# Kernel optimization log

Hardware: AMD Instinct MI355X
Metric: run time of the kernel (lower is better)

## Reference

```python
import jax, jax.numpy as jnp
import numpy as np

CH = 256
C8 = CH // 8


def setup_inputs() -> dict:
    key = jax.random.key(0)
    ks = jax.random.split(key, 8)
    scale = 1.0 / np.sqrt(CH)
    x = jax.random.normal(ks[0], (8, CH, 64, 64), dtype=jnp.float32)
    Wq = jax.random.normal(ks[1], (C8, CH), dtype=jnp.float32) * scale
    bq = jnp.zeros((C8,), dtype=jnp.float32)
    Wk = jax.random.normal(ks[2], (C8, CH), dtype=jnp.float32) * scale
    bk = jnp.zeros((C8,), dtype=jnp.float32)
    Wv = jax.random.normal(ks[3], (CH, CH), dtype=jnp.float32) * scale
    bv = jnp.zeros((CH,), dtype=jnp.float32)
    gamma = jnp.full((1,), 0.1, dtype=jnp.float32)  # nonzero so output depends on attention path
    return {"x": x, "Wq": Wq, "bq": bq, "Wk": Wk, "bk": bk, "Wv": Wv, "bv": bv, "gamma": gamma}


def reference(x, Wq, bq, Wk, bk, Wv, bv, gamma):
    b, c, h, w = x.shape
    hw = h * w
    xf = x.reshape(b, c, hw)  # flatten spatial; 1x1 conv == channel matmul
    q = jnp.einsum('oc,bcn->bno', Wq, xf) + bq          # (b, hw, c/8)
    k = jnp.einsum('oc,bcn->bon', Wk, xf) + bk[None, :, None]  # (b, c/8, hw)
    v = jnp.einsum('oc,bcn->bon', Wv, xf) + bv[None, :, None]  # (b, c, hw)
    attn = jax.nn.softmax(jnp.einsum('bno,bom->bnm', q, k), axis=-1)  # (b, hw, hw)
    out = jnp.einsum('bcm,bnm->bcn', v, attn).reshape(b, c, h, w)
    return x + gamma * out
```

## Files before the change

### kernel.cpp

```cpp
#include <hip/hip_runtime.h>
#include <stdint.h>

constexpr int CHN  = 256;
constexpr int HW   = 4096;
constexpr int QBLK = 64;
constexpr int KVB  = 64;
constexpr int KSTR = 40;
constexpr int VSTR = 72;

typedef float f32x4  __attribute__((ext_vector_type(4)));
typedef short bf16x8 __attribute__((ext_vector_type(8)));
typedef short s16x4  __attribute__((ext_vector_type(4)));

static __device__ __forceinline__ short f2bf(float f) {
  uint32_t u = __builtin_bit_cast(uint32_t, f);
  u += 0x7FFFu + ((u >> 16) & 1u);
  return (short)(u >> 16);
}

__global__ __launch_bounds__(256) void prep_kernel(
    const float* __restrict__ Wq, const float* __restrict__ Wk, const float* __restrict__ Wv,
    const float* __restrict__ bq, const float* __restrict__ bk, const float* __restrict__ bv,
    short* __restrict__ Wb, float* __restrict__ bcat) {
  int idx = blockIdx.x * 256 + threadIdx.x;
  if (idx < 320 * 256) {
    int r = idx >> 8, c = idx & 255;
    float w = (r < 256) ? Wv[idx]
            : (r < 288) ? Wq[(r - 256) * 256 + c]
                        : Wk[(r - 288) * 256 + c];
    Wb[idx] = f2bf(w);
  }
  if (idx < 320)
    bcat[idx] = (idx < 256) ? bv[idx] : (idx < 288) ? bq[idx - 256] : bk[idx - 288];
}

__global__ __launch_bounds__(320) void proj_kernel(
    const float* __restrict__ x, const short* __restrict__ Wb, const float* __restrict__ bcat,
    short* __restrict__ qw, short* __restrict__ kw, short* __restrict__ vw) {
  const int t    = threadIdx.x;
  const int b    = blockIdx.y;
  const int n0   = blockIdx.x * 64;
  const int lane = t & 63;
  const int w    = t >> 6;
  const int ln   = lane & 15;
  const int gp   = lane >> 4;

  const float* xb = x + (size_t)b * CHN * HW + n0;
  const short* wbp = Wb + (w * 64 + ln) * 256 + gp * 8;

  const f32x4 zv = {0.f, 0.f, 0.f, 0.f};
  f32x4 acc[4][4];
#pragma unroll
  for (int i = 0; i < 4; ++i)
#pragma unroll
    for (int j = 0; j < 4; ++j) acc[i][j] = zv;

#pragma unroll 2
  for (int ks = 0; ks < 8; ++ks) {
    const int k0 = ks * 32;
    bf16x8 a[4];
#pragma unroll
    for (int i = 0; i < 4; ++i)
      a[i] = *(const bf16x8*)(wbp + i * 16 * 256 + k0);
    bf16x8 bxv[4];
#pragma unroll
    for (int j = 0; j < 4; ++j) {
      const float* xc = xb + (size_t)(k0 + gp * 8) * HW + 16 * j + ln;
#pragma unroll
      for (int e = 0; e < 8; ++e) bxv[j][e] = f2bf(xc[(size_t)e * HW]);
    }
#pragma unroll
    for (int i = 0; i < 4; ++i)
#pragma unroll
      for (int j = 0; j < 4; ++j)
        acc[i][j] = __builtin_amdgcn_mfma_f32_16x16x32_bf16(a[i], bxv[j], acc[i][j], 0, 0, 0);
  }

  if (w < 4) {
#pragma unroll
    for (int i = 0; i < 4; ++i) {
#pragma unroll
      for (int r = 0; r < 4; ++r) {
        const int o = w * 64 + 16 * i + 4 * gp + r;
        const float bias = bcat[o];
        short* vr = vw + ((size_t)b * CHN + o) * HW + n0 + ln;
#pragma unroll
        for (int j = 0; j < 4; ++j)
          vr[16 * j] = f2bf(acc[i][j][r] + bias);
      }
    }
  } else {
#pragma unroll
    for (int j = 0; j < 4; ++j) {
      const size_t nrow = ((size_t)b * HW + n0 + 16 * j + ln) * 32;
#pragma unroll
      for (int i = 0; i < 2; ++i) {
        s16x4 pq, pk;
#pragma unroll
        for (int r = 0; r < 4; ++r) {
          pq[r] = f2bf(acc[i][j][r]     + bcat[256 + 16 * i + 4 * gp + r]);
          pk[r] = f2bf(acc[i + 2][j][r] + bcat[288 + 16 * i + 4 * gp + r]);
        }
        *(s16x4*)(qw + nrow + 16 * i + 4 * gp) = pq;
        *(s16x4*)(kw + nrow + 16 * i + 4 * gp) = pk;
      }
    }
  }
}

__global__ __launch_bounds__(256, 2) void attn_kernel(
    const float* __restrict__ x, const float* __restrict__ gamma,
    const short* __restrict__ qw, const short* __restrict__ kw, const short* __restrict__ vw,
    float* __restrict__ out) {
  __shared__ union alignas(16) {
    struct { short K[QBLK * KSTR]; short V[CHN * VSTR]; } kv;
    float oc[64 * 65];
  } sm;

  const int tid  = threadIdx.x;
  const int lane = tid & 63;
  const int wv   = tid >> 6;
  const int ln   = lane & 15;
  const int gp   = lane >> 4;
  const int b    = blockIdx.x & 7;
  const int qt   = blockIdx.x >> 3;
  const int qbase = qt * QBLK;

  const short* qb = qw + (size_t)b * HW * 32;
  const short* kb = kw + (size_t)b * HW * 32;
  const short* vb = vw + (size_t)b * CHN * HW;

  const bf16x8 qf = *(const bf16x8*)(qb + (size_t)(qbase + wv * 16 + ln) * 32 + gp * 8);

  const f32x4 zv = {0.f, 0.f, 0.f, 0.f};
  f32x4 O[16];
#pragma unroll
  for (int i = 0; i < 16; ++i) O[i] = zv;
  float mrun = -__builtin_inff();
  float lrun = 0.f;

  for (int kv0 = 0; kv0 < HW; kv0 += KVB) {
    {
      const int row = tid >> 2, ch = tid & 3;
      *(bf16x8*)(&sm.kv.K[row * KSTR + ch * 8]) =
          *(const bf16x8*)(kb + (size_t)(kv0 + row) * 32 + ch * 8);
    }
    {
      const int c0 = tid >> 3, jj = tid & 7;
      const int h = jj >> 2, u = (jj >> 1) & 1, g0 = (jj & 1) * 2;
      const int pos_lo = 32 * h + 8 * g0 + 4 * u;
#pragma unroll
      for (int j = 0; j < 8; ++j) {
        const int c = c0 + j * 32;
        bf16x8 vval = *(const bf16x8*)(vb + (size_t)c * HW + kv0 + jj * 8);
        s16x4 lo = {vval[0], vval[1], vval[2], vval[3]};
        s16x4 hi = {vval[4], vval[5], vval[6], vval[7]};
        *(s16x4*)(&sm.kv.V[c * VSTR + pos_lo])     = lo;
        *(s16x4*)(&sm.kv.V[c * VSTR + pos_lo + 8]) = hi;
      }
    }
    __syncthreads();

    f32x4 st[4];
#pragma unroll
    for (int t2 = 0; t2 < 4; ++t2) {
      bf16x8 kf = *(const bf16x8*)(&sm.kv.K[(t2 * 16 + ln) * KSTR + gp * 8]);
      st[t2] = __builtin_amdgcn_mfma_f32_16x16x32_bf16(kf, qf, zv, 0, 0, 0);
    }

    float tmax = -__builtin_inff();
#pragma unroll
    for (int t2 = 0; t2 < 4; ++t2)
#pragma unroll
      for (int r = 0; r < 4; ++r) tmax = fmaxf(tmax, st[t2][r]);
    tmax = fmaxf(tmax, __shfl_xor(tmax, 16));
    tmax = fmaxf(tmax, __shfl_xor(tmax, 32));
    const float mnew = fmaxf(mrun, tmax);
    const unsigned long long anyup = __ballot(mnew > mrun);
    const float alpha = __expf(mrun - mnew);
    float psum = 0.f;
#pragma unroll
    for (int t2 = 0; t2 < 4; ++t2)
#pragma unroll
      for (int r = 0; r < 4; ++r) {
        float p = __expf(st[t2][r] - mnew);
        st[t2][r] = p;
        psum += p;
      }
    psum += __shfl_xor(psum, 16);
    psum += __shfl_xor(psum, 32);
    lrun = lrun * alpha + psum;
    mrun = mnew;
    if (anyup) {
      float ar[4];
#pragma unroll
      for (int r = 0; r < 4; ++r) ar[r] = __shfl(alpha, gp * 4 + r);
#pragma unroll
      for (int i = 0; i < 16; ++i)
#pragma unroll
        for (int r = 0; r < 4; ++r) O[i][r] *= ar[r];
    }

    bf16x8 pf0, pf1;
#pragma unroll
    for (int i = 0; i < 8; ++i) {
      pf0[i] = f2bf(st[i >> 2][i & 3]);
      pf1[i] = f2bf(st[2 + (i >> 2)][i & 3]);
    }

#pragma unroll
    for (int ct = 0; ct < 16; ++ct) {
      const short* vr = &sm.kv.V[(ct * 16 + ln) * VSTR + gp * 8];
      bf16x8 vf0 = *(const bf16x8*)(vr);
      bf16x8 vf1 = *(const bf16x8*)(vr + 32);
      O[ct] = __builtin_amdgcn_mfma_f32_16x16x32_bf16(pf0, vf0, O[ct], 0, 0, 0);
      O[ct] = __builtin_amdgcn_mfma_f32_16x16x32_bf16(pf1, vf1, O[ct], 0, 0, 0);
    }
    __syncthreads();
  }

  float linv[4];
#pragma unroll
  for (int r = 0; r < 4; ++r) linv[r] = 1.0f / __shfl(lrun, gp * 4 + r);
  const float g0 = gamma[0];

  for (int cc = 0; cc < 4; ++cc) {
    __syncthreads();
#pragma unroll
    for (int j = 0; j < 4; ++j) {
      const int ct = cc * 4 + j;
#pragma unroll
      for (int r = 0; r < 4; ++r)
        sm.oc[(j * 16 + ln) * 65 + (wv * 16 + gp * 4 + r)] = O[ct][r] * linv[r];
    }
    __syncthreads();
#pragma unroll
    for (int rr = 0; rr < 16; ++rr) {
      const int c = cc * 64 + wv * 16 + rr;
      const size_t o = ((size_t)b * CHN + c) * HW + qbase + lane;
      out[o] = x[o] + g0 * sm.oc[(wv * 16 + rr) * 65 + lane];
    }
  }
}

extern "C" void kernel_launch(void* const* d_in, const int* in_sizes, int n_in,
                              void* d_out, int out_size, void* d_ws, size_t ws_size,
                              hipStream_t stream) {
  const float* x     = (const float*)d_in[0];
  const float* Wq    = (const float*)d_in[1];
  const float* bq    = (const float*)d_in[2];
  const float* Wk    = (const float*)d_in[3];
  const float* bk    = (const float*)d_in[4];
  const float* Wv    = (const float*)d_in[5];
  const float* bv    = (const float*)d_in[6];
  const float* gamma = (const float*)d_in[7];
  float* out = (float*)d_out;

  char* ws = (char*)d_ws;
  short* qw   = (short*)(ws);
  short* kw   = (short*)(ws + (2u << 20));
  short* vw   = (short*)(ws + (4u << 20));
  short* Wb   = (short*)(ws + (20u << 20));
  float* bcat = (float*)(ws + (20u << 20) + (256u << 10));

  prep_kernel<<<320, 256, 0, stream>>>(Wq, Wk, Wv, bq, bk, bv, Wb, bcat);
  proj_kernel<<<dim3(64, 8), 320, 0, stream>>>(x, Wb, bcat, qw, kw, vw);
  attn_kernel<<<512, 256, 0, stream>>>(x, gamma, qw, kw, vw, out);
}
```

Baseline: 165.1 us.

## Rewrite attention with 32x32 MFMA, async V staging, exp2 softmax, lazy rescale

The attention kernel is rebuilt around 32x32x16 bf16 MFMA tiles with 128 queries per block. V is stored by the projection kernel in pre-tiled, XOR-swizzled 64-position blobs so it can be streamed into double-buffered LDS with global_load_lds. K fragments are prefetched from global memory straight into registers. The softmax uses exp2, with log2e folded into Q, and only rescales O when the running max grows by more than 8. The epilogue is vectorized. The aim is to overlap loads with MFMA work and to cut exp and rescale costs, at the price of higher register pressure and lower occupancy.

```diff
diff --git a/kernel.cpp b/kernel.cpp
--- a/kernel.cpp
+++ b/kernel.cpp
@@ -1,21 +1,31 @@
 #include <hip/hip_runtime.h>
 #include <stdint.h>
 
-constexpr int CHN  = 256;
-constexpr int HW   = 4096;
-constexpr int QBLK = 64;
-constexpr int KVB  = 64;
-constexpr int KSTR = 40;
-constexpr int VSTR = 72;
-
-typedef float f32x4  __attribute__((ext_vector_type(4)));
-typedef short bf16x8 __attribute__((ext_vector_type(8)));
-typedef short s16x4  __attribute__((ext_vector_type(4)));
+constexpr int CHN = 256;
+constexpr int HW  = 4096;
+
+typedef float f32x4   __attribute__((ext_vector_type(4)));
+typedef float f32x16  __attribute__((ext_vector_type(16)));
+typedef short bf16x8  __attribute__((ext_vector_type(8)));
+typedef short s16x4   __attribute__((ext_vector_type(4)));
+typedef uint32_t u32x4 __attribute__((ext_vector_type(4)));
 
 static __device__ __forceinline__ short f2bf(float f) {
   uint32_t u = __builtin_bit_cast(uint32_t, f);
   u += 0x7FFFu + ((u >> 16) & 1u);
   return (short)(u >> 16);
+}
+
+static __device__ __forceinline__ uint32_t pkbf(float a, float b) {
+  uint32_t r;
+  asm("v_cvt_pk_bf16_f32 %0, %1, %2" : "=v"(r) : "v"(a), "v"(b));
+  return r;
+}
+
+static __device__ __forceinline__ void gl16(const void* g, void* l) {
+  __builtin_amdgcn_global_load_lds(
+      (const __attribute__((address_space(1))) uint32_t*)g,
+      (__attribute__((address_space(3))) uint32_t*)l, 16, 0, 0);
 }
 
 __global__ __launch_bounds__(256) void prep_kernel(
@@ -36,7 +46,7 @@
 
 __global__ __launch_bounds__(320) void proj_kernel(
     const float* __restrict__ x, const short* __restrict__ Wb, const float* __restrict__ bcat,
-    short* __restrict__ qw, short* __restrict__ kw, short* __restrict__ vw) {
+    short* __restrict__ qw, short* __restrict__ kw, short* __restrict__ vws) {
   const int t    = threadIdx.x;
   const int b    = blockIdx.y;
   const int n0   = blockIdx.x * 64;
@@ -45,7 +55,7 @@
   const int ln   = lane & 15;
   const int gp   = lane >> 4;
 
-  const float* xb = x + (size_t)b * CHN * HW + n0;
+  const float* xb  = x + (size_t)b * CHN * HW + n0;
   const short* wbp = Wb + (w * 64 + ln) * 256 + gp * 8;
 
   const f32x4 zv = {0.f, 0.f, 0.f, 0.f};
@@ -77,19 +87,22 @@
   }
 
   if (w < 4) {
+    short* vblob = vws + ((size_t)(b * 64 + blockIdx.x)) * 16384;
+    const int ph = 8 * ((ln >> 2) & 1) + 4 * (ln >> 3) + (ln & 3);
 #pragma unroll
     for (int i = 0; i < 4; ++i) {
 #pragma unroll
       for (int r = 0; r < 4; ++r) {
-        const int o = w * 64 + 16 * i + 4 * gp + r;
-        const float bias = bcat[o];
-        short* vr = vw + ((size_t)b * CHN + o) * HW + n0 + ln;
+        const int c = w * 64 + 16 * i + 4 * gp + r;
+        const float bias = bcat[c];
+        const int sw = (c & 7) << 3;
 #pragma unroll
         for (int j = 0; j < 4; ++j)
-          vr[16 * j] = f2bf(acc[i][j][r] + bias);
+          vblob[c * 64 + ((16 * j + ph) ^ sw)] = f2bf(acc[i][j][r] + bias);
       }
     }
   } else {
+    constexpr float LOG2E = 1.44269504088896340736f;
 #pragma unroll
     for (int j = 0; j < 4; ++j) {
       const size_t nrow = ((size_t)b * HW + n0 + 16 * j + ln) * 32;
@@ -98,7 +111,7 @@
         s16x4 pq, pk;
 #pragma unroll
         for (int r = 0; r < 4; ++r) {
-          pq[r] = f2bf(acc[i][j][r]     + bcat[256 + 16 * i + 4 * gp + r]);
+          pq[r] = f2bf((acc[i][j][r] + bcat[256 + 16 * i + 4 * gp + r]) * LOG2E);
           pk[r] = f2bf(acc[i + 2][j][r] + bcat[288 + 16 * i + 4 * gp + r]);
         }
         *(s16x4*)(qw + nrow + 16 * i + 4 * gp) = pq;
@@ -108,137 +121,145 @@
   }
 }
 
-__global__ __launch_bounds__(256, 2) void attn_kernel(
+__global__ __launch_bounds__(256, 1) void attn_kernel(
     const float* __restrict__ x, const float* __restrict__ gamma,
-    const short* __restrict__ qw, const short* __restrict__ kw, const short* __restrict__ vw,
-    float* __restrict__ out) {
-  __shared__ union alignas(16) {
-    struct { short K[QBLK * KSTR]; short V[CHN * VSTR]; } kv;
-    float oc[64 * 65];
-  } sm;
+    const short* __restrict__ qw, const short* __restrict__ kw,
+    const short* __restrict__ vws, float* __restrict__ out) {
+  __shared__ alignas(16) char sm[2 * 32768];
 
   const int tid  = threadIdx.x;
   const int lane = tid & 63;
   const int wv   = tid >> 6;
-  const int ln   = lane & 15;
-  const int gp   = lane >> 4;
+  const int l5   = lane & 31;
+  const int h    = lane >> 5;
   const int b    = blockIdx.x & 7;
   const int qt   = blockIdx.x >> 3;
-  const int qbase = qt * QBLK;
-
-  const short* qb = qw + (size_t)b * HW * 32;
-  const short* kb = kw + (size_t)b * HW * 32;
-  const short* vb = vw + (size_t)b * CHN * HW;
-
-  const bf16x8 qf = *(const bf16x8*)(qb + (size_t)(qbase + wv * 16 + ln) * 32 + gp * 8);
-
-  const f32x4 zv = {0.f, 0.f, 0.f, 0.f};
-  f32x4 O[16];
-#pragma unroll
-  for (int i = 0; i < 16; ++i) O[i] = zv;
-  float mrun = -__builtin_inff();
-  float lrun = 0.f;
-
-  for (int kv0 = 0; kv0 < HW; kv0 += KVB) {
-    {
-      const int row = tid >> 2, ch = tid & 3;
-      *(bf16x8*)(&sm.kv.K[row * KSTR + ch * 8]) =
-          *(const bf16x8*)(kb + (size_t)(kv0 + row) * 32 + ch * 8);
-    }
-    {
-      const int c0 = tid >> 3, jj = tid & 7;
-      const int h = jj >> 2, u = (jj >> 1) & 1, g0 = (jj & 1) * 2;
-      const int pos_lo = 32 * h + 8 * g0 + 4 * u;
-#pragma unroll
-      for (int j = 0; j < 8; ++j) {
-        const int c = c0 + j * 32;
-        bf16x8 vval = *(const bf16x8*)(vb + (size_t)c * HW + kv0 + jj * 8);
-        s16x4 lo = {vval[0], vval[1], vval[2], vval[3]};
-        s16x4 hi = {vval[4], vval[5], vval[6], vval[7]};
-        *(s16x4*)(&sm.kv.V[c * VSTR + pos_lo])     = lo;
-        *(s16x4*)(&sm.kv.V[c * VSTR + pos_lo + 8]) = hi;
-      }
-    }
+  const int qbase = qt * 128;
+
+  const short* qb    = qw + (size_t)b * HW * 32;
+  const short* kb    = kw + (size_t)b * HW * 32;
+  const char*  vblob = (const char*)vws + (size_t)b * 64 * 32768;
+
+  const short* qrow = qb + (size_t)(qbase + wv * 32 + l5) * 32 + h * 8;
+  const bf16x8 qf0 = *(const bf16x8*)(qrow);
+  const bf16x8 qf1 = *(const bf16x8*)(qrow + 16);
+
+  f32x16 z16;
+#pragma unroll
+  for (int r = 0; r < 16; ++r) z16[r] = 0.f;
+  f32x16 O[8];
+#pragma unroll
+  for (int ct = 0; ct < 8; ++ct) O[ct] = z16;
+
+  float mrun = -1e30f, lrun = 0.f;
+
+  {
+    const char* gs = vblob + (wv * 8) * 1024 + lane * 16;
+    char* ld = sm + (wv * 8) * 1024;
+#pragma unroll
+    for (int j = 0; j < 8; ++j) gl16(gs + j * 1024, ld + j * 1024);
+  }
+
+  const short* kfb = kb + (size_t)l5 * 32 + h * 8;
+  bf16x8 kf00 = *(const bf16x8*)(kfb);
+  bf16x8 kf01 = *(const bf16x8*)(kfb + 16);
+  bf16x8 kf10 = *(const bf16x8*)(kfb + 1024);
+  bf16x8 kf11 = *(const bf16x8*)(kfb + 1024 + 16);
+
+  const int swv = (l5 & 7) << 4;
+
+  for (int it = 0; it < 64; ++it) {
     __syncthreads();
-
-    f32x4 st[4];
-#pragma unroll
-    for (int t2 = 0; t2 < 4; ++t2) {
-      bf16x8 kf = *(const bf16x8*)(&sm.kv.K[(t2 * 16 + ln) * KSTR + gp * 8]);
-      st[t2] = __builtin_amdgcn_mfma_f32_16x16x32_bf16(kf, qf, zv, 0, 0, 0);
-    }
-
-    float tmax = -__builtin_inff();
-#pragma unroll
-    for (int t2 = 0; t2 < 4; ++t2)
-#pragma unroll
-      for (int r = 0; r < 4; ++r) tmax = fmaxf(tmax, st[t2][r]);
-    tmax = fmaxf(tmax, __shfl_xor(tmax, 16));
+    const char* buf = sm + (it & 1) * 32768;
+    if (it < 63) {
+      const char* gs = vblob + (size_t)(it + 1) * 32768 + (wv * 8) * 1024 + lane * 16;
+      char* ld = sm + ((it + 1) & 1) * 32768 + (wv * 8) * 1024;
+#pragma unroll
+      for (int j = 0; j < 8; ++j) gl16(gs + j * 1024, ld + j * 1024);
+    }
+
+    f32x16 s0 = __builtin_amdgcn_mfma_f32_32x32x16_bf16(kf00, qf0, z16, 0, 0, 0);
+    s0 = __builtin_amdgcn_mfma_f32_32x32x16_bf16(kf01, qf1, s0, 0, 0, 0);
+    f32x16 s1 = __builtin_amdgcn_mfma_f32_32x32x16_bf16(kf10, qf0, z16, 0, 0, 0);
+    s1 = __builtin_amdgcn_mfma_f32_32x32x16_bf16(kf11, qf1, s1, 0, 0, 0);
+
+    if (it < 63) {
+      const short* kn = kfb + (size_t)(it + 1) * 2048;
+      kf00 = *(const bf16x8*)(kn);
+      kf01 = *(const bf16x8*)(kn + 16);
+      kf10 = *(const bf16x8*)(kn + 1024);
+      kf11 = *(const bf16x8*)(kn + 1024 + 16);
+    }
+
+    float tmax = -1e30f;
+#pragma unroll
+    for (int r = 0; r < 16; ++r) tmax = fmaxf(tmax, fmaxf(s0[r], s1[r]));
     tmax = fmaxf(tmax, __shfl_xor(tmax, 32));
-    const float mnew = fmaxf(mrun, tmax);
-    const unsigned long long anyup = __ballot(mnew > mrun);
-    const float alpha = __expf(mrun - mnew);
-    float psum = 0.f;
-#pragma unroll
-    for (int t2 = 0; t2 < 4; ++t2)
-#pragma unroll
-      for (int r = 0; r < 4; ++r) {
-        float p = __expf(st[t2][r] - mnew);
-        st[t2][r] = p;
-        psum += p;
-      }
-    psum += __shfl_xor(psum, 16);
-    psum += __shfl_xor(psum, 32);
-    lrun = lrun * alpha + psum;
-    mrun = mnew;
-    if (anyup) {
-      float ar[4];
-#pragma unroll
-      for (int r = 0; r < 4; ++r) ar[r] = __shfl(alpha, gp * 4 + r);
-#pragma unroll
-      for (int i = 0; i < 16; ++i)
-#pragma unroll
-        for (int r = 0; r < 4; ++r) O[i][r] *= ar[r];
-    }
-
-    bf16x8 pf0, pf1;
-#pragma unroll
-    for (int i = 0; i < 8; ++i) {
-      pf0[i] = f2bf(st[i >> 2][i & 3]);
-      pf1[i] = f2bf(st[2 + (i >> 2)][i & 3]);
-    }
-
-#pragma unroll
-    for (int ct = 0; ct < 16; ++ct) {
-      const short* vr = &sm.kv.V[(ct * 16 + ln) * VSTR + gp * 8];
-      bf16x8 vf0 = *(const bf16x8*)(vr);
-      bf16x8 vf1 = *(const bf16x8*)(vr + 32);
-      O[ct] = __builtin_amdgcn_mfma_f32_16x16x32_bf16(pf0, vf0, O[ct], 0, 0, 0);
-      O[ct] = __builtin_amdgcn_mfma_f32_16x16x32_bf16(pf1, vf1, O[ct], 0, 0, 0);
-    }
+    if (__any(tmax > mrun + 8.f)) {
+      const float mnew = fmaxf(mrun, tmax);
+      const float al = __builtin_amdgcn_exp2f(mrun - mnew);
+      lrun *= al;
+      mrun = mnew;
+#pragma unroll
+      for (int r = 0; r < 16; ++r) {
+        const float ar = __shfl(al, (r & 3) + ((r >> 2) << 3) + (h << 2));
+#pragma unroll
+        for (int ct = 0; ct < 8; ++ct) O[ct][r] *= ar;
+      }
+    }
+    float ps = 0.f;
+#pragma unroll
+    for (int r = 0; r < 16; ++r) {
+      s0[r] = __builtin_amdgcn_exp2f(s0[r] - mrun);
+      s1[r] = __builtin_amdgcn_exp2f(s1[r] - mrun);
+      ps += s0[r] + s1[r];
+    }
+    ps += __shfl_xor(ps, 32);
+    lrun += ps;
+
+    const char* vb0 = buf + l5 * 128;
+#pragma unroll
+    for (int mt = 0; mt < 4; ++mt) {
+      const int r0 = (mt & 1) * 8;
+      uint32_t w0, w1, w2, w3;
+      if (mt < 2) {
+        w0 = pkbf(s0[r0 + 0], s0[r0 + 1]); w1 = pkbf(s0[r0 + 2], s0[r0 + 3]);
+        w2 = pkbf(s0[r0 + 4], s0[r0 + 5]); w3 = pkbf(s0[r0 + 6], s0[r0 + 7]);
+      } else {
+        w0 = pkbf(s1[r0 + 0], s1[r0 + 1]); w1 = pkbf(s1[r0 + 2], s1[r0 + 3]);
+        w2 = pkbf(s1[r0 + 4], s1[r0 + 5]); w3 = pkbf(s1[r0 + 6], s1[r0 + 7]);
+      }
+      const u32x4 paw = {w0, w1, w2, w3};
+      const bf16x8 pa = __builtin_bit_cast(bf16x8, paw);
+      const char* vbm = vb0 + ((32 * mt + 16 * h) ^ swv);
+#pragma unroll
+      for (int ct = 0; ct < 8; ++ct) {
+        const bf16x8 vf = *(const bf16x8*)(vbm + ct * 4096);
+        O[ct] = __builtin_amdgcn_mfma_f32_32x32x16_bf16(pa, vf, O[ct], 0, 0, 0);
+      }
+    }
+  }
+
+  const float g0 = gamma[0];
+  float linv[16];
+#pragma unroll
+  for (int r = 0; r < 16; ++r)
+    linv[r] = g0 / __shfl(lrun, (r & 3) + ((r >> 2) << 3) + (h << 2));
+
+  float* eo = (float*)sm;
+  for (int ct = 0; ct < 8; ++ct) {
     __syncthreads();
-  }
-
-  float linv[4];
-#pragma unroll
-  for (int r = 0; r < 4; ++r) linv[r] = 1.0f / __shfl(lrun, gp * 4 + r);
-  const float g0 = gamma[0];
-
-  for (int cc = 0; cc < 4; ++cc) {
+#pragma unroll
+    for (int r = 0; r < 16; ++r)
+      eo[l5 * 132 + wv * 32 + ((r & 3) + ((r >> 2) << 3) + (h << 2))] = O[ct][r] * linv[r];
     __syncthreads();
-#pragma unroll
-    for (int j = 0; j < 4; ++j) {
-      const int ct = cc * 4 + j;
-#pragma unroll
-      for (int r = 0; r < 4; ++r)
-        sm.oc[(j * 16 + ln) * 65 + (wv * 16 + gp * 4 + r)] = O[ct][r] * linv[r];
-    }
-    __syncthreads();
-#pragma unroll
-    for (int rr = 0; rr < 16; ++rr) {
-      const int c = cc * 64 + wv * 16 + rr;
-      const size_t o = ((size_t)b * CHN + c) * HW + qbase + lane;
-      out[o] = x[o] + g0 * sm.oc[(wv * 16 + rr) * 65 + lane];
+    const int cl = tid >> 3, seg = tid & 7;
+    const size_t gi = ((size_t)b * CHN + ct * 32 + cl) * HW + qbase + seg * 16;
+#pragma unroll
+    for (int u = 0; u < 4; ++u) {
+      const f32x4 xv = *(const f32x4*)(x + gi + u * 4);
+      const f32x4 ov = *(const f32x4*)(&eo[cl * 132 + seg * 16 + u * 4]);
+      *(f32x4*)(out + gi + u * 4) = xv + ov;
     }
   }
 }
@@ -259,11 +280,11 @@
   char* ws = (char*)d_ws;
   short* qw   = (short*)(ws);
   short* kw   = (short*)(ws + (2u << 20));
-  short* vw   = (short*)(ws + (4u << 20));
+  short* vws  = (short*)(ws + (4u << 20));
   short* Wb   = (short*)(ws + (20u << 20));
   float* bcat = (float*)(ws + (20u << 20) + (256u << 10));
 
   prep_kernel<<<320, 256, 0, stream>>>(Wq, Wk, Wv, bq, bk, bv, Wb, bcat);
-  proj_kernel<<<dim3(64, 8), 320, 0, stream>>>(x, Wb, bcat, qw, kw, vw);
-  attn_kernel<<<512, 256, 0, stream>>>(x, gamma, qw, kw, vw, out);
-}
+  proj_kernel<<<dim3(64, 8), 320, 0, stream>>>(x, Wb, bcat, qw, kw, vws);
+  attn_kernel<<<256, 256, 0, stream>>>(x, gamma, qw, kw, vws, out);
+}
```

Result: faster. 153.7 us (-6.9%).
